# Optimization experiments

Measured on AMD Instinct MI355X. Metric: run time of the kernel, lower is better.

## Reference

```python
import jax, jax.numpy as jnp
import numpy as np

VOC_SIZE = 100000
EMB_SIZE = 300
BATCH = 262144


def setup_inputs() -> dict:
    key = jax.random.key(0)
    k1, k2, k3, k4, k5, k6, k7, k8 = jax.random.split(key, 8)
    center = jax.random.randint(k1, (BATCH, 1), 0, VOC_SIZE)
    outside = jax.random.randint(k2, (BATCH, 1), 0, VOC_SIZE)
    coocs = jax.random.uniform(k3, (BATCH, 1), dtype=jnp.float32)
    weighting = jax.random.uniform(k4, (BATCH, 1), dtype=jnp.float32)
    center_embedding = jax.random.normal(k5, (VOC_SIZE, EMB_SIZE), dtype=jnp.float32)
    outside_embedding = jax.random.normal(k6, (VOC_SIZE, EMB_SIZE), dtype=jnp.float32)
    center_bias = jax.random.normal(k7, (VOC_SIZE, 1), dtype=jnp.float32)
    outside_bias = jax.random.normal(k8, (VOC_SIZE, 1), dtype=jnp.float32)
    return {
        "center": center,
        "outside": outside,
        "coocs": coocs,
        "weighting": weighting,
        "center_embedding": center_embedding,
        "outside_embedding": outside_embedding,
        "center_bias": center_bias,
        "outside_bias": outside_bias,
    }


def reference(center, outside, coocs, weighting,
              center_embedding, outside_embedding,
              center_bias, outside_bias):
    c_idx = center[:, 0]    # [B]
    o_idx = outside[:, 0]   # [B]
    center_embeds = center_embedding[c_idx]     # [B, E]
    outside_embeds = outside_embedding[o_idx]   # [B, E]
    c_bias = center_bias[c_idx]                 # [B, 1]
    o_bias = outside_bias[o_idx]                # [B, 1]
    # per-sample dot product, keepdims to match [B, 1]
    inner = jnp.sum(center_embeds * outside_embeds, axis=-1, keepdims=True)  # [B, 1]
    err = inner + c_bias + o_bias - coocs
    loss = jnp.sum(weighting * err * err)
    return loss
```

## Files before the change

kernel.cpp:

```cpp
#include <hip/hip_runtime.h>

#define GLOVE_BATCH 262144
#define EMB 300
#define VEC4 (EMB / 4)

__global__ void glove_zero_out(float* out) {
    if (threadIdx.x == 0 && blockIdx.x == 0) out[0] = 0.0f;
}

__global__ __launch_bounds__(256) void glove_loss_kernel(
    const int*   __restrict__ center,
    const int*   __restrict__ outside,
    const float* __restrict__ coocs,
    const float* __restrict__ weighting,
    const float* __restrict__ cemb,
    const float* __restrict__ oemb,
    const float* __restrict__ cbias,
    const float* __restrict__ obias,
    float*       __restrict__ out)
{
    const int lane    = threadIdx.x & 63;
    const int warp    = threadIdx.x >> 6;
    const int wave_id = blockIdx.x * 4 + warp;
    const int n_waves = gridDim.x * 4;

    float local = 0.0f;

    for (int p = wave_id; p < GLOVE_BATCH; p += n_waves) {
        const int ci = center[p];
        const int oi = outside[p];
        const float4* __restrict__ ca = (const float4*)(cemb + (long)ci * EMB);
        const float4* __restrict__ ob = (const float4*)(oemb + (long)oi * EMB);

        float acc = 0.0f;
        {
            float4 a = ca[lane];
            float4 b = ob[lane];
            acc += a.x * b.x + a.y * b.y + a.z * b.z + a.w * b.w;
        }
        if (lane < VEC4 - 64) {
            float4 a = ca[lane + 64];
            float4 b = ob[lane + 64];
            acc += a.x * b.x + a.y * b.y + a.z * b.z + a.w * b.w;
        }

        #pragma unroll
        for (int off = 32; off > 0; off >>= 1)
            acc += __shfl_down(acc, off, 64);

        if (lane == 0) {
            const float err = acc + cbias[ci] + obias[oi] - coocs[p];
            local += weighting[p] * err * err;
        }
    }

    __shared__ float smem[4];
    if (lane == 0) smem[warp] = local;
    __syncthreads();
    if (threadIdx.x == 0) {
        const float s = smem[0] + smem[1] + smem[2] + smem[3];
        atomicAdd(out, s);
    }
}

extern "C" void kernel_launch(void* const* d_in, const int* in_sizes, int n_in,
                              void* d_out, int out_size, void* d_ws, size_t ws_size,
                              hipStream_t stream) {
    const int*   center    = (const int*)  d_in[0];
    const int*   outside   = (const int*)  d_in[1];
    const float* coocs     = (const float*)d_in[2];
    const float* weighting = (const float*)d_in[3];
    const float* cemb      = (const float*)d_in[4];
    const float* oemb      = (const float*)d_in[5];
    const float* cbias     = (const float*)d_in[6];
    const float* obias     = (const float*)d_in[7];
    float* out = (float*)d_out;

    glove_zero_out<<<1, 64, 0, stream>>>(out);

    glove_loss_kernel<<<8192, 256, 0, stream>>>(
        center, outside, coocs, weighting, cemb, oemb, cbias, obias, out);
}
```

Baseline: 363.7 us.

## Batch four pairs per wave for memory-level parallelism and replace atomics with two-pass reduction

Each wave now processes a contiguous chunk of 16 pairs in groups of four. It issues all index, bias and embedding-row loads for a group before doing the interleaved shuffle reductions, so more gathers are in flight at once. The atomicAdd into a zeroed output is replaced by per-block partial sums in workspace plus a single-block final reduction kernel, which also removes the zeroing launch. In exchange, register pressure rises, the ws buffer is assumed to hold 4096 floats, and the work split is hardcoded to the batch size.

```diff
diff --git a/kernel.cpp b/kernel.cpp
--- a/kernel.cpp
+++ b/kernel.cpp
@@ -1,14 +1,13 @@
 #include <hip/hip_runtime.h>
 
-#define GLOVE_BATCH 262144
+#define BATCH 262144
 #define EMB 300
-#define VEC4 (EMB / 4)
+#define NBLK 4096
+#define WPB 4
+#define PAIRS_PER_WAVE 16
+#define UNROLL 4
 
-__global__ void glove_zero_out(float* out) {
-    if (threadIdx.x == 0 && blockIdx.x == 0) out[0] = 0.0f;
-}
-
-__global__ __launch_bounds__(256) void glove_loss_kernel(
+__global__ __launch_bounds__(256) void glove_main(
     const int*   __restrict__ center,
     const int*   __restrict__ outside,
     const float* __restrict__ coocs,
@@ -17,49 +16,88 @@
     const float* __restrict__ oemb,
     const float* __restrict__ cbias,
     const float* __restrict__ obias,
-    float*       __restrict__ out)
+    float*       __restrict__ block_sums)
 {
-    const int lane    = threadIdx.x & 63;
-    const int warp    = threadIdx.x >> 6;
-    const int wave_id = blockIdx.x * 4 + warp;
-    const int n_waves = gridDim.x * 4;
+    const int lane = threadIdx.x & 63;
+    const int warp = threadIdx.x >> 6;
+    const int wave_base = (blockIdx.x * WPB + warp) * PAIRS_PER_WAVE;
 
     float local = 0.0f;
 
-    for (int p = wave_id; p < GLOVE_BATCH; p += n_waves) {
-        const int ci = center[p];
-        const int oi = outside[p];
-        const float4* __restrict__ ca = (const float4*)(cemb + (long)ci * EMB);
-        const float4* __restrict__ ob = (const float4*)(oemb + (long)oi * EMB);
+    #pragma unroll
+    for (int it = 0; it < PAIRS_PER_WAVE / UNROLL; ++it) {
+        const int p0 = wave_base + it * UNROLL;
 
-        float acc = 0.0f;
-        {
-            float4 a = ca[lane];
-            float4 b = ob[lane];
-            acc += a.x * b.x + a.y * b.y + a.z * b.z + a.w * b.w;
-        }
-        if (lane < VEC4 - 64) {
-            float4 a = ca[lane + 64];
-            float4 b = ob[lane + 64];
-            acc += a.x * b.x + a.y * b.y + a.z * b.z + a.w * b.w;
-        }
+        int   ci[UNROLL], oi[UNROLL];
+        float cb[UNROLL], ob2[UNROLL], cc[UNROLL], wt[UNROLL];
+        float acc[UNROLL];
 
         #pragma unroll
-        for (int off = 32; off > 0; off >>= 1)
-            acc += __shfl_down(acc, off, 64);
-
+        for (int j = 0; j < UNROLL; ++j) {
+            ci[j] = center[p0 + j];
+            oi[j] = outside[p0 + j];
+        }
+        #pragma unroll
+        for (int j = 0; j < UNROLL; ++j) {
+            cc[j]  = coocs[p0 + j];
+            wt[j]  = weighting[p0 + j];
+            cb[j]  = cbias[ci[j]];
+            ob2[j] = obias[oi[j]];
+        }
+        #pragma unroll
+        for (int j = 0; j < UNROLL; ++j) {
+            const float4* __restrict__ A = (const float4*)(cemb + (long)ci[j] * EMB);
+            const float4* __restrict__ B = (const float4*)(oemb + (long)oi[j] * EMB);
+            float4 a = A[lane];
+            float4 b = B[lane];
+            float s = a.x * b.x + a.y * b.y + a.z * b.z + a.w * b.w;
+            if (lane < 11) {
+                float4 a2 = A[lane + 64];
+                float4 b2 = B[lane + 64];
+                s += a2.x * b2.x + a2.y * b2.y + a2.z * b2.z + a2.w * b2.w;
+            }
+            acc[j] = s;
+        }
+        #pragma unroll
+        for (int off = 32; off > 0; off >>= 1) {
+            #pragma unroll
+            for (int j = 0; j < UNROLL; ++j)
+                acc[j] += __shfl_down(acc[j], off, 64);
+        }
         if (lane == 0) {
-            const float err = acc + cbias[ci] + obias[oi] - coocs[p];
-            local += weighting[p] * err * err;
+            #pragma unroll
+            for (int j = 0; j < UNROLL; ++j) {
+                const float e = acc[j] + cb[j] + ob2[j] - cc[j];
+                local += wt[j] * e * e;
+            }
         }
     }
 
-    __shared__ float smem[4];
+    __shared__ float smem[WPB];
     if (lane == 0) smem[warp] = local;
     __syncthreads();
-    if (threadIdx.x == 0) {
-        const float s = smem[0] + smem[1] + smem[2] + smem[3];
-        atomicAdd(out, s);
+    if (threadIdx.x == 0)
+        block_sums[blockIdx.x] = smem[0] + smem[1] + smem[2] + smem[3];
+}
+
+__global__ __launch_bounds__(1024) void glove_reduce(
+    const float* __restrict__ part, float* __restrict__ out)
+{
+    const int t = threadIdx.x;
+    float4 v = ((const float4*)part)[t];
+    float s = v.x + v.y + v.z + v.w;
+    #pragma unroll
+    for (int off = 32; off > 0; off >>= 1)
+        s += __shfl_down(s, off, 64);
+    __shared__ float sm[16];
+    if ((t & 63) == 0) sm[t >> 6] = s;
+    __syncthreads();
+    if (t < 16) {
+        float x = sm[t];
+        #pragma unroll
+        for (int off = 8; off > 0; off >>= 1)
+            x += __shfl_down(x, off, 16);
+        if (t == 0) out[0] = x;
     }
 }
 
@@ -74,10 +112,10 @@
     const float* oemb      = (const float*)d_in[5];
     const float* cbias     = (const float*)d_in[6];
     const float* obias     = (const float*)d_in[7];
-    float* out = (float*)d_out;
+    float* out        = (float*)d_out;
+    float* block_sums = (float*)d_ws;
 
-    glove_zero_out<<<1, 64, 0, stream>>>(out);
-
-    glove_loss_kernel<<<8192, 256, 0, stream>>>(
-        center, outside, coocs, weighting, cemb, oemb, cbias, obias, out);
+    glove_main<<<NBLK, 256, 0, stream>>>(
+        center, outside, coocs, weighting, cemb, oemb, cbias, obias, block_sums);
+    glove_reduce<<<1, 1024, 0, stream>>>(block_sums, out);
 }
```

After: 309.2 us. 15.0% less time.
